# Kernel optimization log

Measured on AMD Instinct MI355X. Metric: run time of the kernel, lower is better.

Reference implementation:

```python
import jax, jax.numpy as jnp
import numpy as np

B, L, D = 4, 4096, 128
BLOCK, SPARSITY = 64, 0.9
NEG = -1e9


def _make_block_mask(key):
    nb = L // BLOCK
    bm = jax.random.uniform(key, (nb, nb)) > SPARSITY
    bm = bm | jnp.eye(nb, dtype=bool)  # keep diagonal blocks so no row is fully masked
    bm = jnp.tril(bm)
    return jnp.repeat(jnp.repeat(bm, BLOCK, axis=0), BLOCK, axis=1)  # [L, L]


def _xavier(key, shape):
    limit = float(np.sqrt(6.0 / (shape[0] + shape[1])))
    return jax.random.uniform(key, shape, jnp.float32, -limit, limit)


def setup_inputs() -> dict:
    key = jax.random.key(0)
    ks = jax.random.split(key, 10)
    t = lambda k: jax.random.normal(k, (B, L, D), jnp.float32)
    return {
        'q_real': t(ks[0]), 'q_imag': t(ks[1]),
        'k_real': t(ks[2]), 'k_imag': t(ks[3]),
        'v_real': t(ks[4]), 'v_imag': t(ks[5]),
        'W_qkv': _xavier(ks[6], (6 * D, 6 * D)),
        'b_qkv': jnp.zeros((6 * D,), jnp.float32),
        'W_out': _xavier(ks[7], (2 * D, 2 * D)),
        'b_out': jnp.zeros((2 * D,), jnp.float32),
        'block_mask': _make_block_mask(ks[8]),
    }


def reference(q_real, q_imag, k_real, k_imag, v_real, v_imag,
              W_qkv, b_qkv, W_out, b_out, block_mask):
    d = q_real.shape[-1]
    scale = d ** -0.5
    # fused qkv projection over the 6 concatenated channels
    x = jnp.concatenate([q_real, q_imag, k_real, k_imag, v_real, v_imag], axis=-1)  # [B,L,6D]
    qkv = (x @ W_qkv.T + b_qkv).reshape(x.shape[0], x.shape[1], 6, d)
    q_r, q_i, k_r, k_i, v_r, v_i = (qkv[:, :, j] for j in range(6))

    def attn(q, k, v):
        s = jnp.einsum('bqd,bkd->bqk', q, k) * scale          # [B,L,L]
        s = jnp.where(block_mask[None], s, NEG)               # block-sparse mask
        a = jax.nn.softmax(s, axis=-1)                        # dropout = identity (eval)
        return jnp.einsum('bqk,bkd->bqd', a, v)

    out = jnp.concatenate([attn(q_r, k_r, v_r), attn(q_i, k_i, v_i)], axis=-1)  # [B,L,2D]
    out = out @ W_out.T + b_out
    return out[..., :d], out[..., d:]
```

## Files before the change

### kernel.cpp

```cpp
#include <hip/hip_runtime.h>
#include <hip/hip_bf16.h>

typedef unsigned short u16;
typedef __attribute__((ext_vector_type(8))) short bf16x8;
typedef __attribute__((ext_vector_type(4))) float f32x4;

#define SEQ_L 4096
#define M_TOT 16384

__device__ __forceinline__ float bf2f(u16 x) {
    unsigned u = ((unsigned)x) << 16;
    return __builtin_bit_cast(float, u);
}
__device__ __forceinline__ u16 f2bf(float f) {
    unsigned u = __builtin_bit_cast(unsigned, f);
    u += 0x7FFFu + ((u >> 16) & 1u);
    return (u16)(u >> 16);
}
__device__ __forceinline__ void gload16(const u16* g, u16* l) {
    __builtin_amdgcn_global_load_lds(
        (const __attribute__((address_space(1))) unsigned int*)g,
        (__attribute__((address_space(3))) unsigned int*)l, 16, 0, 0);
}

__global__ __launch_bounds__(256) void prep_all(
    const float* __restrict__ in0, const float* __restrict__ in1, const float* __restrict__ in2,
    const float* __restrict__ in3, const float* __restrict__ in4, const float* __restrict__ in5,
    const float* __restrict__ Wqkv, const float* __restrict__ Wout, const void* __restrict__ mask,
    u16* __restrict__ x, u16* __restrict__ Wqkv_bf, u16* __restrict__ Wout_bf,
    unsigned char* __restrict__ cmask) {
    int id = blockIdx.x * 256 + threadIdx.x;
    if (id < 1572864) {
        const float* ins[6] = {in0, in1, in2, in3, in4, in5};
        int which = id >> 18, j = id & 262143;
        int m = j >> 4, c8 = j & 15;
        const float* sp = ins[which] + (size_t)m * 128 + c8 * 8;
        float4 a = *(const float4*)sp;
        float4 b = *(const float4*)(sp + 4);
        u16 t[8] = {f2bf(a.x), f2bf(a.y), f2bf(a.z), f2bf(a.w),
                    f2bf(b.x), f2bf(b.y), f2bf(b.z), f2bf(b.w)};
        *(uint4*)(x + (size_t)m * 768 + which * 128 + c8 * 8) = *(uint4*)t;
    } else if (id < 1572864 + 73728 + 8192) {
        int i = id - 1572864;
        const float* src = (i < 73728) ? Wqkv : Wout;
        u16* dst = (i < 73728) ? Wqkv_bf : Wout_bf;
        if (i >= 73728) i -= 73728;
        const float* sp = src + (size_t)i * 8;
        float4 a = *(const float4*)sp;
        float4 b = *(const float4*)(sp + 4);
        u16 t[8] = {f2bf(a.x), f2bf(a.y), f2bf(a.z), f2bf(a.w),
                    f2bf(b.x), f2bf(b.y), f2bf(b.z), f2bf(b.w)};
        *(uint4*)(dst + (size_t)i * 8) = *(uint4*)t;
    } else if (id < 1572864 + 73728 + 8192 + 4096) {
        int i = id - 1572864 - 73728 - 8192;
        int bi = i >> 6, bj = i & 63;
        size_t e = (size_t)(bi * 64) * SEQ_L + (size_t)bj * 64;
        const unsigned char* p8 = (const unsigned char*)mask;
        unsigned w0 = *(const unsigned*)mask;
        bool v;
        if (w0 == 0x01010101u || w0 == 0xFFFFFFFFu)      v = p8[e] != 0;
        else if (w0 == 0x3F803F80u || w0 == 0x3C003C00u) v = ((const u16*)mask)[e] != 0;
        else                                             v = ((const unsigned*)mask)[e] != 0;
        cmask[i] = v ? 1 : 0;
    }
}

__global__ __launch_bounds__(256) void qkv_gemm(
    const u16* __restrict__ X, const u16* __restrict__ W, const float* __restrict__ bias,
    u16* __restrict__ qk, u16* __restrict__ vt) {
    __shared__ __align__(16) u16 As[128 * 64];
    __shared__ __align__(16) u16 Bs[128 * 64];
    int m0 = blockIdx.x * 128, n0 = blockIdx.y * 128;
    int tid = threadIdx.x, lane = tid & 63, w = tid >> 6;
    int ln = lane & 15, quad = lane >> 4;
    int rw = (w >> 1) * 64, cw = (w & 1) * 64;
    int lr8 = lane >> 3, lc = lane & 7;
    int swz_st = lc ^ (lr8 & 7);
    f32x4 acc[4][4] = {};
    for (int kk = 0; kk < 768; kk += 64) {
        __syncthreads();
        #pragma unroll
        for (int j = 0; j < 4; j++) {
            int r0 = w * 32 + j * 8;
            int r = r0 + lr8;
            gload16(X + (size_t)(m0 + r) * 768 + kk + swz_st * 8, As + r0 * 64 + lane * 8);
            gload16(W + (size_t)(n0 + r) * 768 + kk + swz_st * 8, Bs + r0 * 64 + lane * 8);
        }
        __syncthreads();
        #pragma unroll
        for (int s = 0; s < 2; s++) {
            bf16x8 af[4], bfr[4];
            #pragma unroll
            for (int i = 0; i < 4; i++) {
                int R = rw + i * 16 + ln;
                af[i] = *(const bf16x8*)(As + R * 64 + ((4 * s + quad) ^ (ln & 7)) * 8);
            }
            #pragma unroll
            for (int t = 0; t < 4; t++) {
                int R = cw + t * 16 + ln;
                bfr[t] = *(const bf16x8*)(Bs + R * 64 + ((4 * s + quad) ^ (ln & 7)) * 8);
            }
            #pragma unroll
            for (int i = 0; i < 4; i++)
                #pragma unroll
                for (int t = 0; t < 4; t++)
                    acc[i][t] = __builtin_amdgcn_mfma_f32_16x16x32_bf16(af[i], bfr[t], acc[i][t], 0, 0, 0);
        }
    }
    #pragma unroll
    for (int i = 0; i < 4; i++) {
        int row0 = m0 + rw + i * 16 + 4 * quad;
        #pragma unroll
        for (int t = 0; t < 4; t++) {
            int col = n0 + cw + t * 16 + ln;
            float bv = bias[col];
            if (col < 512) {
                #pragma unroll
                for (int r = 0; r < 4; r++)
                    qk[(size_t)(row0 + r) * 512 + col] = f2bf(acc[i][t][r] + bv);
            } else {
                int d = col - 512;
                int b = row0 >> 12, seq = row0 & 4095;
                u16 pk[4] = {f2bf(acc[i][t][0] + bv), f2bf(acc[i][t][1] + bv),
                             f2bf(acc[i][t][2] + bv), f2bf(acc[i][t][3] + bv)};
                *(ushort4*)(vt + ((size_t)(b * 2 + (d >> 7)) * 128 + (d & 127)) * SEQ_L + seq)
                    = *(ushort4*)pk;
            }
        }
    }
}

__global__ __launch_bounds__(256) void attn_out(
    const u16* __restrict__ qk, const u16* __restrict__ vt, const u16* __restrict__ Wout,
    const unsigned char* __restrict__ cmask, const float* __restrict__ bout,
    float* __restrict__ out) {
    __shared__ __align__(16) u16 Ks[2][64 * 128];
    __shared__ __align__(16) u16 Vt[2][128 * 64];
    __shared__ __align__(16) u16 Ps[4][16 * 72];
    __shared__ __align__(16) u16 Ao[64 * 264];

    int idx = blockIdx.x;
    int qi = 63 - (idx >> 2);
    int b = idx & 3;
    int tid = threadIdx.x, lane = tid & 63, w = tid >> 6;
    int ln = lane & 15, quad = lane >> 4;
    const float scale = 0.08838834764831845f;

    int k_lr = lane >> 4, k_lc = lane & 15;
    int v_lr = lane >> 3, v_lc = lane & 7;

    const unsigned char* mrow = cmask + qi * 64;
    unsigned long long bm0 = 0;
    for (int k = 0; k <= qi; k++) bm0 |= (unsigned long long)(mrow[k] != 0) << k;

    for (int c = 0; c < 2; c++) {
        const u16* kb_base = qk + (size_t)b * SEQ_L * 512 + 256 + c * 128;
        const u16* vt_base = vt + (size_t)(b * 2 + c) * 128 * SEQ_L;

        bf16x8 qf[4];
        {
            size_t grow = (size_t)(b * SEQ_L + qi * 64 + w * 16 + ln);
            const u16* qp = qk + grow * 512 + c * 128;
            #pragma unroll
            for (int s = 0; s < 4; s++) qf[s] = *(const bf16x8*)(qp + 32 * s + 8 * quad);
        }
        float m_st[4], l_st[4];
        #pragma unroll
        for (int r = 0; r < 4; r++) { m_st[r] = -1e30f; l_st[r] = 0.f; }
        f32x4 accO[8] = {};

        unsigned long long bm = bm0;
        int cur = __ffsll(bm) - 1; bm &= bm - 1;
        int buf = 0;
        __syncthreads();
        {
            const u16* kp = kb_base + (size_t)cur * 64 * 512;
            const u16* vp = vt_base + cur * 64;
            #pragma unroll
            for (int j = 0; j < 4; j++) {
                int kr0 = w * 16 + j * 4, kr = kr0 + k_lr;
                gload16(kp + (size_t)kr * 512 + (k_lc ^ (kr & 7)) * 8, Ks[0] + kr0 * 128 + lane * 8);
                int vr0 = w * 32 + j * 8, vr = vr0 + v_lr;
                gload16(vp + (size_t)vr * SEQ_L + (v_lc ^ (vr & 7)) * 8, Vt[0] + vr0 * 64 + lane * 8);
            }
        }
        while (cur >= 0) {
            int nxt = bm ? (__ffsll(bm) - 1) : -1;
            if (bm) bm &= bm - 1;
            __syncthreads();
            if (nxt >= 0) {
                const u16* kp = kb_base + (size_t)nxt * 64 * 512;
                const u16* vp = vt_base + nxt * 64;
                #pragma unroll
                for (int j = 0; j < 4; j++) {
                    int kr0 = w * 16 + j * 4, kr = kr0 + k_lr;
                    gload16(kp + (size_t)kr * 512 + (k_lc ^ (kr & 7)) * 8, Ks[buf ^ 1] + kr0 * 128 + lane * 8);
                    int vr0 = w * 32 + j * 8, vr = vr0 + v_lr;
                    gload16(vp + (size_t)vr * SEQ_L + (v_lc ^ (vr & 7)) * 8, Vt[buf ^ 1] + vr0 * 64 + lane * 8);
                }
            }

            f32x4 accS[4] = {};
            #pragma unroll
            for (int s = 0; s < 4; s++) {
                #pragma unroll
                for (int t = 0; t < 4; t++) {
                    int R = t * 16 + ln;
                    bf16x8 bfr = *(const bf16x8*)(Ks[buf] + R * 128 + ((4 * s + quad) ^ (ln & 7)) * 8);
                    accS[t] = __builtin_amdgcn_mfma_f32_16x16x32_bf16(qf[s], bfr, accS[t], 0, 0, 0);
                }
            }
            float P[4][4];
            #pragma unroll
            for (int r = 0; r < 4; r++) {
                float sv[4];
                float mx = -1e30f;
                #pragma unroll
                for (int t = 0; t < 4; t++) { sv[t] = accS[t][r] * scale; mx = fmaxf(mx, sv[t]); }
                #pragma unroll
                for (int off = 1; off < 16; off <<= 1) mx = fmaxf(mx, __shfl_xor(mx, off, 64));
                float nm = fmaxf(m_st[r], mx);
                float alpha = __expf(m_st[r] - nm);
                m_st[r] = nm;
                float rs = 0.f;
                #pragma unroll
                for (int t = 0; t < 4; t++) { float p = __expf(sv[t] - nm); P[t][r] = p; rs += p; }
                #pragma unroll
                for (int off = 1; off < 16; off <<= 1) rs += __shfl_xor(rs, off, 64);
                l_st[r] = l_st[r] * alpha + rs;
                #pragma unroll
                for (int nt = 0; nt < 8; nt++) accO[nt][r] *= alpha;
            }
            #pragma unroll
            for (int t = 0; t < 4; t++)
                #pragma unroll
                for (int r = 0; r < 4; r++)
                    Ps[w][(4 * quad + r) * 72 + ln + 16 * t] = f2bf(P[t][r]);
            #pragma unroll
            for (int s2 = 0; s2 < 2; s2++) {
                bf16x8 pf = *(const bf16x8*)(&Ps[w][ln * 72 + 32 * s2 + 8 * quad]);
                #pragma unroll
                for (int nt = 0; nt < 8; nt++) {
                    int R = nt * 16 + ln;
                    bf16x8 vf = *(const bf16x8*)(Vt[buf] + R * 64 + ((4 * s2 + quad) ^ (ln & 7)) * 8);
                    accO[nt] = __builtin_amdgcn_mfma_f32_16x16x32_bf16(pf, vf, accO[nt], 0, 0, 0);
                }
            }
            cur = nxt; buf ^= 1;
        }
        float inv[4];
        #pragma unroll
        for (int r = 0; r < 4; r++) inv[r] = 1.0f / fmaxf(l_st[r], 1e-20f);
        #pragma unroll
        for (int nt = 0; nt < 8; nt++)
            #pragma unroll
            for (int r = 0; r < 4; r++)
                Ao[(w * 16 + 4 * quad + r) * 264 + c * 128 + nt * 16 + ln]
                    = f2bf(accO[nt][r] * inv[r]);
    }

    u16* Bs = Ks[0];
    f32x4 oacc[4][4] = {};
    for (int kk = 0; kk < 4; kk++) {
        __syncthreads();
        #pragma unroll
        for (int j = 0; j < 8; j++) {
            int o0 = w * 64 + j * 8;
            int o = o0 + (lane >> 3);
            gload16(Wout + (size_t)o * 256 + kk * 64 + (((lane & 7) ^ (o & 7)) * 8),
                    Bs + o0 * 64 + lane * 8);
        }
        __syncthreads();
        #pragma unroll
        for (int s = 0; s < 2; s++) {
            bf16x8 af[4], bfr[4];
            #pragma unroll
            for (int i = 0; i < 4; i++)
                af[i] = *(const bf16x8*)(Ao + (i * 16 + ln) * 264 + kk * 64 + 32 * s + 8 * quad);
            #pragma unroll
            for (int t = 0; t < 4; t++) {
                int o = w * 64 + t * 16 + ln;
                bfr[t] = *(const bf16x8*)(Bs + o * 64 + ((4 * s + quad) ^ (ln & 7)) * 8);
            }
            #pragma unroll
            for (int i = 0; i < 4; i++)
                #pragma unroll
                for (int t = 0; t < 4; t++)
                    oacc[i][t] = __builtin_amdgcn_mfma_f32_16x16x32_bf16(af[i], bfr[t], oacc[i][t], 0, 0, 0);
        }
    }
    const size_t half = (size_t)M_TOT * 128;
    #pragma unroll
    for (int t = 0; t < 4; t++) {
        int o = w * 64 + t * 16 + ln;
        float bv = bout[o];
        float* base = (o < 128) ? (out + o) : (out + half + (o - 128));
        #pragma unroll
        for (int i = 0; i < 4; i++) {
            int row = b * SEQ_L + qi * 64 + i * 16 + 4 * quad;
            #pragma unroll
            for (int r = 0; r < 4; r++)
                base[(size_t)(row + r) * 128] = oacc[i][t][r] + bv;
        }
    }
}

extern "C" void kernel_launch(void* const* d_in, const int* in_sizes, int n_in,
                              void* d_out, int out_size, void* d_ws, size_t ws_size,
                              hipStream_t stream) {
    char* ws = (char*)d_ws;
    u16* x_bf    = (u16*)ws;
    u16* qk_buf  = x_bf + (size_t)M_TOT * 768;
    u16* vt_buf  = qk_buf + (size_t)M_TOT * 512;
    u16* Wqkv_bf = vt_buf + (size_t)1024 * SEQ_L;
    u16* Wout_bf = Wqkv_bf + 589824;
    unsigned char* cmask = (unsigned char*)(Wout_bf + 65536);

    hipLaunchKernelGGL(prep_all, dim3(6480), dim3(256), 0, stream,
                       (const float*)d_in[0], (const float*)d_in[1], (const float*)d_in[2],
                       (const float*)d_in[3], (const float*)d_in[4], (const float*)d_in[5],
                       (const float*)d_in[6], (const float*)d_in[8], d_in[10],
                       x_bf, Wqkv_bf, Wout_bf, cmask);
    hipLaunchKernelGGL(qkv_gemm, dim3(128, 6), dim3(256), 0, stream,
                       x_bf, Wqkv_bf, (const float*)d_in[7], qk_buf, vt_buf);
    hipLaunchKernelGGL(attn_out, dim3(256), dim3(256), 0, stream,
                       qk_buf, vt_buf, Wout_bf, cmask, (const float*)d_in[9], (float*)d_out);
}
```

Before: 242.8 us.

## Split attention blocks across query halves and channels; narrow QKV GEMM tiles

The attention kernel now launches 512 blocks instead of 256. Each block handles 32 query rows, and its waves split the real and imaginary channels in parallel instead of looping over them one after the other. The K/V double-buffering is dropped in favour of a single load followed by a sync on each sparse block, and the P scratch and output tiles now share one LDS region. The QKV GEMM uses 128x64 tiles with a 4-blocks-per-CU launch bound, which doubles its grid. The aim is more parallelism on the 256-CU device, at the cost of losing load/compute overlap and loading Wout twice as often.

```diff
diff --git a/kernel.cpp b/kernel.cpp
--- a/kernel.cpp
+++ b/kernel.cpp
@@ -65,45 +65,47 @@
     }
 }
 
-__global__ __launch_bounds__(256) void qkv_gemm(
+__global__ __launch_bounds__(256, 4) void qkv_gemm(
     const u16* __restrict__ X, const u16* __restrict__ W, const float* __restrict__ bias,
     u16* __restrict__ qk, u16* __restrict__ vt) {
     __shared__ __align__(16) u16 As[128 * 64];
-    __shared__ __align__(16) u16 Bs[128 * 64];
-    int m0 = blockIdx.x * 128, n0 = blockIdx.y * 128;
+    __shared__ __align__(16) u16 Bs[64 * 64];
+    int m0 = blockIdx.x * 128, n0 = blockIdx.y * 64;
     int tid = threadIdx.x, lane = tid & 63, w = tid >> 6;
     int ln = lane & 15, quad = lane >> 4;
-    int rw = (w >> 1) * 64, cw = (w & 1) * 64;
+    int rw = (w >> 1) * 64, cw = (w & 1) * 32;
     int lr8 = lane >> 3, lc = lane & 7;
-    int swz_st = lc ^ (lr8 & 7);
-    f32x4 acc[4][4] = {};
+    f32x4 acc[4][2] = {};
     for (int kk = 0; kk < 768; kk += 64) {
         __syncthreads();
         #pragma unroll
         for (int j = 0; j < 4; j++) {
-            int r0 = w * 32 + j * 8;
-            int r = r0 + lr8;
-            gload16(X + (size_t)(m0 + r) * 768 + kk + swz_st * 8, As + r0 * 64 + lane * 8);
-            gload16(W + (size_t)(n0 + r) * 768 + kk + swz_st * 8, Bs + r0 * 64 + lane * 8);
+            int r0 = w * 32 + j * 8, r = r0 + lr8;
+            gload16(X + (size_t)(m0 + r) * 768 + kk + ((lc ^ (r & 7)) * 8), As + r0 * 64 + lane * 8);
+        }
+        #pragma unroll
+        for (int j = 0; j < 2; j++) {
+            int r0 = w * 16 + j * 8, r = r0 + lr8;
+            gload16(W + (size_t)(n0 + r) * 768 + kk + ((lc ^ (r & 7)) * 8), Bs + r0 * 64 + lane * 8);
         }
         __syncthreads();
         #pragma unroll
         for (int s = 0; s < 2; s++) {
-            bf16x8 af[4], bfr[4];
+            bf16x8 af[4], bfr[2];
             #pragma unroll
             for (int i = 0; i < 4; i++) {
                 int R = rw + i * 16 + ln;
                 af[i] = *(const bf16x8*)(As + R * 64 + ((4 * s + quad) ^ (ln & 7)) * 8);
             }
             #pragma unroll
-            for (int t = 0; t < 4; t++) {
+            for (int t = 0; t < 2; t++) {
                 int R = cw + t * 16 + ln;
                 bfr[t] = *(const bf16x8*)(Bs + R * 64 + ((4 * s + quad) ^ (ln & 7)) * 8);
             }
             #pragma unroll
             for (int i = 0; i < 4; i++)
                 #pragma unroll
-                for (int t = 0; t < 4; t++)
+                for (int t = 0; t < 2; t++)
                     acc[i][t] = __builtin_amdgcn_mfma_f32_16x16x32_bf16(af[i], bfr[t], acc[i][t], 0, 0, 0);
         }
     }
@@ -111,7 +113,7 @@
     for (int i = 0; i < 4; i++) {
         int row0 = m0 + rw + i * 16 + 4 * quad;
         #pragma unroll
-        for (int t = 0; t < 4; t++) {
+        for (int t = 0; t < 2; t++) {
             int col = n0 + cw + t * 16 + ln;
             float bv = bias[col];
             if (col < 512) {
@@ -136,118 +138,104 @@
     float* __restrict__ out) {
     __shared__ __align__(16) u16 Ks[2][64 * 128];
     __shared__ __align__(16) u16 Vt[2][128 * 64];
-    __shared__ __align__(16) u16 Ps[4][16 * 72];
-    __shared__ __align__(16) u16 Ao[64 * 264];
+    __shared__ __align__(16) u16 PsAo[32 * 256];
 
     int idx = blockIdx.x;
-    int qi = 63 - (idx >> 2);
-    int b = idx & 3;
+    int qi = 63 - (idx >> 3);
+    int b = (idx >> 1) & 3, half = idx & 1;
     int tid = threadIdx.x, lane = tid & 63, w = tid >> 6;
     int ln = lane & 15, quad = lane >> 4;
+    int cw = w >> 1, wr = w & 1;
     const float scale = 0.08838834764831845f;
 
-    int k_lr = lane >> 4, k_lc = lane & 15;
-    int v_lr = lane >> 3, v_lc = lane & 7;
-
     const unsigned char* mrow = cmask + qi * 64;
-    unsigned long long bm0 = 0;
-    for (int k = 0; k <= qi; k++) bm0 |= (unsigned long long)(mrow[k] != 0) << k;
-
-    for (int c = 0; c < 2; c++) {
-        const u16* kb_base = qk + (size_t)b * SEQ_L * 512 + 256 + c * 128;
-        const u16* vt_base = vt + (size_t)(b * 2 + c) * 128 * SEQ_L;
-
-        bf16x8 qf[4];
-        {
-            size_t grow = (size_t)(b * SEQ_L + qi * 64 + w * 16 + ln);
-            const u16* qp = qk + grow * 512 + c * 128;
-            #pragma unroll
-            for (int s = 0; s < 4; s++) qf[s] = *(const bf16x8*)(qp + 32 * s + 8 * quad);
-        }
-        float m_st[4], l_st[4];
-        #pragma unroll
-        for (int r = 0; r < 4; r++) { m_st[r] = -1e30f; l_st[r] = 0.f; }
-        f32x4 accO[8] = {};
-
-        unsigned long long bm = bm0;
+    unsigned long long bm = 0;
+    for (int k = 0; k <= qi; k++) bm |= (unsigned long long)(mrow[k] != 0) << k;
+
+    const u16* kb_base = qk + (size_t)b * SEQ_L * 512 + 256 + cw * 128;
+    const u16* vt_base = vt + (size_t)(b * 2 + cw) * 128 * SEQ_L;
+
+    bf16x8 qf[4];
+    {
+        size_t grow = (size_t)(b * SEQ_L + qi * 64 + half * 32 + wr * 16 + ln);
+        const u16* qp = qk + grow * 512 + cw * 128;
+        #pragma unroll
+        for (int s = 0; s < 4; s++) qf[s] = *(const bf16x8*)(qp + 32 * s + 8 * quad);
+    }
+    float m_st[4], l_st[4];
+    #pragma unroll
+    for (int r = 0; r < 4; r++) { m_st[r] = -1e30f; l_st[r] = 0.f; }
+    f32x4 accO[8] = {};
+    u16* Ps = PsAo + w * 1152;
+
+    while (bm) {
         int cur = __ffsll(bm) - 1; bm &= bm - 1;
-        int buf = 0;
         __syncthreads();
         {
             const u16* kp = kb_base + (size_t)cur * 64 * 512;
             const u16* vp = vt_base + cur * 64;
             #pragma unroll
-            for (int j = 0; j < 4; j++) {
-                int kr0 = w * 16 + j * 4, kr = kr0 + k_lr;
-                gload16(kp + (size_t)kr * 512 + (k_lc ^ (kr & 7)) * 8, Ks[0] + kr0 * 128 + lane * 8);
-                int vr0 = w * 32 + j * 8, vr = vr0 + v_lr;
-                gload16(vp + (size_t)vr * SEQ_L + (v_lc ^ (vr & 7)) * 8, Vt[0] + vr0 * 64 + lane * 8);
-            }
-        }
-        while (cur >= 0) {
-            int nxt = bm ? (__ffsll(bm) - 1) : -1;
-            if (bm) bm &= bm - 1;
-            __syncthreads();
-            if (nxt >= 0) {
-                const u16* kp = kb_base + (size_t)nxt * 64 * 512;
-                const u16* vp = vt_base + nxt * 64;
-                #pragma unroll
-                for (int j = 0; j < 4; j++) {
-                    int kr0 = w * 16 + j * 4, kr = kr0 + k_lr;
-                    gload16(kp + (size_t)kr * 512 + (k_lc ^ (kr & 7)) * 8, Ks[buf ^ 1] + kr0 * 128 + lane * 8);
-                    int vr0 = w * 32 + j * 8, vr = vr0 + v_lr;
-                    gload16(vp + (size_t)vr * SEQ_L + (v_lc ^ (vr & 7)) * 8, Vt[buf ^ 1] + vr0 * 64 + lane * 8);
-                }
-            }
-
-            f32x4 accS[4] = {};
-            #pragma unroll
-            for (int s = 0; s < 4; s++) {
-                #pragma unroll
-                for (int t = 0; t < 4; t++) {
-                    int R = t * 16 + ln;
-                    bf16x8 bfr = *(const bf16x8*)(Ks[buf] + R * 128 + ((4 * s + quad) ^ (ln & 7)) * 8);
-                    accS[t] = __builtin_amdgcn_mfma_f32_16x16x32_bf16(qf[s], bfr, accS[t], 0, 0, 0);
-                }
-            }
-            float P[4][4];
-            #pragma unroll
-            for (int r = 0; r < 4; r++) {
-                float sv[4];
-                float mx = -1e30f;
-                #pragma unroll
-                for (int t = 0; t < 4; t++) { sv[t] = accS[t][r] * scale; mx = fmaxf(mx, sv[t]); }
-                #pragma unroll
-                for (int off = 1; off < 16; off <<= 1) mx = fmaxf(mx, __shfl_xor(mx, off, 64));
-                float nm = fmaxf(m_st[r], mx);
-                float alpha = __expf(m_st[r] - nm);
-                m_st[r] = nm;
-                float rs = 0.f;
-                #pragma unroll
-                for (int t = 0; t < 4; t++) { float p = __expf(sv[t] - nm); P[t][r] = p; rs += p; }
-                #pragma unroll
-                for (int off = 1; off < 16; off <<= 1) rs += __shfl_xor(rs, off, 64);
-                l_st[r] = l_st[r] * alpha + rs;
-                #pragma unroll
-                for (int nt = 0; nt < 8; nt++) accO[nt][r] *= alpha;
-            }
-            #pragma unroll
-            for (int t = 0; t < 4; t++)
-                #pragma unroll
-                for (int r = 0; r < 4; r++)
-                    Ps[w][(4 * quad + r) * 72 + ln + 16 * t] = f2bf(P[t][r]);
-            #pragma unroll
-            for (int s2 = 0; s2 < 2; s2++) {
-                bf16x8 pf = *(const bf16x8*)(&Ps[w][ln * 72 + 32 * s2 + 8 * quad]);
-                #pragma unroll
-                for (int nt = 0; nt < 8; nt++) {
-                    int R = nt * 16 + ln;
-                    bf16x8 vf = *(const bf16x8*)(Vt[buf] + R * 64 + ((4 * s2 + quad) ^ (ln & 7)) * 8);
-                    accO[nt] = __builtin_amdgcn_mfma_f32_16x16x32_bf16(pf, vf, accO[nt], 0, 0, 0);
-                }
-            }
-            cur = nxt; buf ^= 1;
-        }
+            for (int j = 0; j < 8; j++) {
+                int kr0 = j * 8 + wr * 4, kr = kr0 + (lane >> 4);
+                gload16(kp + (size_t)kr * 512 + (((lane & 15) ^ (kr & 7)) * 8),
+                        Ks[cw] + kr0 * 128 + lane * 8);
+                int d0 = j * 16 + wr * 8, d = d0 + (lane >> 3);
+                gload16(vp + (size_t)d * SEQ_L + (((lane & 7) ^ (d & 7)) * 8),
+                        Vt[cw] + d0 * 64 + lane * 8);
+            }
+        }
+        __syncthreads();
+
+        f32x4 accS[4] = {};
+        #pragma unroll
+        for (int s = 0; s < 4; s++) {
+            #pragma unroll
+            for (int t = 0; t < 4; t++) {
+                int R = t * 16 + ln;
+                bf16x8 bfr = *(const bf16x8*)(Ks[cw] + R * 128 + ((4 * s + quad) ^ (ln & 7)) * 8);
+                accS[t] = __builtin_amdgcn_mfma_f32_16x16x32_bf16(qf[s], bfr, accS[t], 0, 0, 0);
+            }
+        }
+        float P[4][4];
+        #pragma unroll
+        for (int r = 0; r < 4; r++) {
+            float sv[4];
+            float mx = -1e30f;
+            #pragma unroll
+            for (int t = 0; t < 4; t++) { sv[t] = accS[t][r] * scale; mx = fmaxf(mx, sv[t]); }
+            #pragma unroll
+            for (int off = 1; off < 16; off <<= 1) mx = fmaxf(mx, __shfl_xor(mx, off, 64));
+            float nm = fmaxf(m_st[r], mx);
+            float alpha = __expf(m_st[r] - nm);
+            m_st[r] = nm;
+            float rs = 0.f;
+            #pragma unroll
+            for (int t = 0; t < 4; t++) { float p = __expf(sv[t] - nm); P[t][r] = p; rs += p; }
+            #pragma unroll
+            for (int off = 1; off < 16; off <<= 1) rs += __shfl_xor(rs, off, 64);
+            l_st[r] = l_st[r] * alpha + rs;
+            #pragma unroll
+            for (int nt = 0; nt < 8; nt++) accO[nt][r] *= alpha;
+        }
+        #pragma unroll
+        for (int t = 0; t < 4; t++)
+            #pragma unroll
+            for (int r = 0; r < 4; r++)
+                Ps[(4 * quad + r) * 72 + ln + 16 * t] = f2bf(P[t][r]);
+        #pragma unroll
+        for (int s2 = 0; s2 < 2; s2++) {
+            bf16x8 pf = *(const bf16x8*)(Ps + ln * 72 + 32 * s2 + 8 * quad);
+            #pragma unroll
+            for (int nt = 0; nt < 8; nt++) {
+                int R = nt * 16 + ln;
+                bf16x8 vf = *(const bf16x8*)(Vt[cw] + R * 64 + ((4 * s2 + quad) ^ (ln & 7)) * 8);
+                accO[nt] = __builtin_amdgcn_mfma_f32_16x16x32_bf16(pf, vf, accO[nt], 0, 0, 0);
+            }
+        }
+    }
+
+    __syncthreads();
+    {
         float inv[4];
         #pragma unroll
         for (int r = 0; r < 4; r++) inv[r] = 1.0f / fmaxf(l_st[r], 1e-20f);
@@ -255,49 +243,48 @@
         for (int nt = 0; nt < 8; nt++)
             #pragma unroll
             for (int r = 0; r < 4; r++)
-                Ao[(w * 16 + 4 * quad + r) * 264 + c * 128 + nt * 16 + ln]
+                PsAo[(wr * 16 + 4 * quad + r) * 256 + cw * 128 + nt * 16 + ln]
                     = f2bf(accO[nt][r] * inv[r]);
     }
 
     u16* Bs = Ks[0];
-    f32x4 oacc[4][4] = {};
+    f32x4 oacc[2][4] = {};
     for (int kk = 0; kk < 4; kk++) {
         __syncthreads();
         #pragma unroll
         for (int j = 0; j < 8; j++) {
-            int o0 = w * 64 + j * 8;
-            int o = o0 + (lane >> 3);
+            int o0 = w * 64 + j * 8, o = o0 + (lane >> 3);
             gload16(Wout + (size_t)o * 256 + kk * 64 + (((lane & 7) ^ (o & 7)) * 8),
                     Bs + o0 * 64 + lane * 8);
         }
         __syncthreads();
         #pragma unroll
         for (int s = 0; s < 2; s++) {
-            bf16x8 af[4], bfr[4];
-            #pragma unroll
-            for (int i = 0; i < 4; i++)
-                af[i] = *(const bf16x8*)(Ao + (i * 16 + ln) * 264 + kk * 64 + 32 * s + 8 * quad);
+            bf16x8 af[2], bfr[4];
+            #pragma unroll
+            for (int i = 0; i < 2; i++)
+                af[i] = *(const bf16x8*)(PsAo + (i * 16 + ln) * 256 + kk * 64 + 32 * s + 8 * quad);
             #pragma unroll
             for (int t = 0; t < 4; t++) {
                 int o = w * 64 + t * 16 + ln;
                 bfr[t] = *(const bf16x8*)(Bs + o * 64 + ((4 * s + quad) ^ (ln & 7)) * 8);
             }
             #pragma unroll
-            for (int i = 0; i < 4; i++)
+            for (int i = 0; i < 2; i++)
                 #pragma unroll
                 for (int t = 0; t < 4; t++)
                     oacc[i][t] = __builtin_amdgcn_mfma_f32_16x16x32_bf16(af[i], bfr[t], oacc[i][t], 0, 0, 0);
         }
     }
-    const size_t half = (size_t)M_TOT * 128;
+    const size_t hlf = (size_t)M_TOT * 128;
     #pragma unroll
     for (int t = 0; t < 4; t++) {
         int o = w * 64 + t * 16 + ln;
         float bv = bout[o];
-        float* base = (o < 128) ? (out + o) : (out + half + (o - 128));
-        #pragma unroll
-        for (int i = 0; i < 4; i++) {
-            int row = b * SEQ_L + qi * 64 + i * 16 + 4 * quad;
+        float* base = (o < 128) ? (out + o) : (out + hlf + (o - 128));
+        #pragma unroll
+        for (int i = 0; i < 2; i++) {
+            int row = b * SEQ_L + qi * 64 + half * 32 + i * 16 + 4 * quad;
             #pragma unroll
             for (int r = 0; r < 4; r++)
                 base[(size_t)(row + r) * 128] = oacc[i][t][r] + bv;
@@ -321,8 +308,8 @@
                        (const float*)d_in[3], (const float*)d_in[4], (const float*)d_in[5],
                        (const float*)d_in[6], (const float*)d_in[8], d_in[10],
                        x_bf, Wqkv_bf, Wout_bf, cmask);
-    hipLaunchKernelGGL(qkv_gemm, dim3(128, 6), dim3(256), 0, stream,
+    hipLaunchKernelGGL(qkv_gemm, dim3(128, 12), dim3(256), 0, stream,
                        x_bf, Wqkv_bf, (const float*)d_in[7], qk_buf, vt_buf);
-    hipLaunchKernelGGL(attn_out, dim3(256), dim3(256), 0, stream,
+    hipLaunchKernelGGL(attn_out, dim3(512), dim3(256), 0, stream,
                        qk_buf, vt_buf, Wout_bf, cmask, (const float*)d_in[9], (float*)d_out);
 }
```

Result: faster. 219.7 us (-9.5%).
